# Performance work log

Measured on AMD Instinct MI355X. Metric: run time of the kernel, lower is better.

The kernel has to match this reference:

```python
import jax, jax.numpy as jnp
import numpy as np

B, S, D, H = 2, 2048, 1024, 16
DH = D // H  # 64, matches Attention's hardcoded d_k=64 scale


def setup_inputs() -> dict:
    key = jax.random.key(0)
    kq, kk, kv, kw, kb = jax.random.split(key, 5)
    return {
        "q": jax.random.normal(kq, (B, S, D), dtype=jnp.float32),
        "k": jax.random.normal(kk, (B, S, D), dtype=jnp.float32),
        "v": jax.random.normal(kv, (B, S, D), dtype=jnp.float32),
        "w_o_w": jax.random.normal(kw, (D, D), dtype=jnp.float32) * 0.02,
        "w_o_b": jax.random.normal(kb, (D,), dtype=jnp.float32) * 0.02,
    }


def _to_heads(x):
    # [B,S,D] -> [B,H,S,DH]
    b, s, d = x.shape
    return x.reshape(b, s, H, DH).transpose(0, 2, 1, 3)


def reference(q, k, v, w_o_w, w_o_b):
    # pre-activation (F.relu) on raw q,k,v
    qh = _to_heads(jax.nn.relu(q))
    kh = _to_heads(jax.nn.relu(k))
    vh = _to_heads(jax.nn.relu(v))
    scale = 1.0 / jnp.sqrt(jnp.asarray(DH, dtype=q.dtype))
    # naive attention: full [B,H,S,S] score matrix, softmax over keys
    scores = jnp.einsum("bhsd,bhtd->bhst", qh, kh) * scale
    probs = jax.nn.softmax(scores, axis=-1)
    attn = jnp.einsum("bhst,bhtd->bhsd", probs, vh)
    # merge heads: [B,H,S,DH] -> [B,S,D]
    out = attn.transpose(0, 2, 1, 3).reshape(B, S, D)
    # output projection (nn.Linear applies x @ W.T + b) then post-activation
    out = out @ w_o_w.T + w_o_b
    return jax.nn.relu(out)
```

## Files before the change

### kernel.cpp

```cpp
#include <hip/hip_runtime.h>
#include <hip/hip_bf16.h>

#define Bc 2
#define Hc 16
#define Sc 2048
#define Dc 1024

typedef __attribute__((ext_vector_type(8))) short s16x8;
typedef __attribute__((ext_vector_type(4))) float f32x4;
typedef __attribute__((ext_vector_type(16))) float f32x16;

#define AS1 __attribute__((address_space(1)))
#define AS3 __attribute__((address_space(3)))

static __device__ __forceinline__ int swz(int row) {
    return (row & 7) ^ ((row >> 3) & 3);
}

static __device__ __forceinline__ float fexp2(float x) {
#if __has_builtin(__builtin_amdgcn_exp2f)
    return __builtin_amdgcn_exp2f(x);
#else
    float r; asm("v_exp_f32 %0, %1" : "=v"(r) : "v"(x)); return r;
#endif
}

static __device__ __forceinline__ unsigned cvtpk(float lo, float hi) {
    unsigned r; asm("v_cvt_pk_bf16_f32 %0, %1, %2" : "=v"(r) : "v"(lo), "v"(hi));
    return r;
}

static __device__ __forceinline__ void plswap(unsigned &x, unsigned &y) {
#if __has_builtin(__builtin_amdgcn_permlane32_swap)
    typedef __attribute__((ext_vector_type(2))) unsigned int u32x2;
    u32x2 t = __builtin_amdgcn_permlane32_swap(x, y, false, false);
    x = t.x; y = t.y;
#else
    asm volatile("v_permlane32_swap_b32 %0, %1" : "+v"(x), "+v"(y));
#endif
}

static __device__ __forceinline__ unsigned short f2bf(float f) {
    union { float f; unsigned u; } x; x.f = f;
    unsigned r = x.u + 0x7fffu + ((x.u >> 16) & 1u);
    return (unsigned short)(r >> 16);
}

__global__ __launch_bounds__(256) void prep_all(const float* __restrict__ q,
                                                const float* __restrict__ k,
                                                const float* __restrict__ v,
                                                const float* __restrict__ w,
                                                unsigned short* __restrict__ qh,
                                                unsigned short* __restrict__ kh,
                                                unsigned short* __restrict__ vt,
                                                unsigned short* __restrict__ wb) {
    const int bid = blockIdx.x;
    const int tid = threadIdx.x;
    if (bid < 8192) {
        const bool isQ = bid < 4096;
        const float* src = isQ ? q : k;
        unsigned short* dst = isQ ? qh : kh;
        const float scale = isQ ? 0.18033688011112042f : 1.0f;
        long i = ((long)(bid & 4095) * 256 + tid) * 4;
        int dh = (int)(i & 63);
        int h  = (int)((i >> 6) & (Hc - 1));
        int s  = (int)((i >> 10) & (Sc - 1));
        int b  = (int)(i >> 21);
        float4 x = *reinterpret_cast<const float4*>(src + i);
        long o = (((long)b * Hc + h) * Sc + s) * 64 + dh;
        ushort4 r;
        r.x = f2bf(fmaxf(x.x, 0.f) * scale);
        r.y = f2bf(fmaxf(x.y, 0.f) * scale);
        r.z = f2bf(fmaxf(x.z, 0.f) * scale);
        r.w = f2bf(fmaxf(x.w, 0.f) * scale);
        *reinterpret_cast<ushort4*>(dst + o) = r;
    } else if (bid < 9216) {
        __shared__ unsigned short lds[64][66];
        const int lb = bid - 8192;
        const int st = lb & (Sc / 64 - 1);
        const int bh = lb >> 5;
        const int b = bh >> 4, h = bh & 15;
#pragma unroll
        for (int i = 0; i < 4; ++i) {
            int srow = (tid >> 4) + i * 16;
            int scol = (tid & 15) * 4;
            float4 x = *(const float4*)(v + ((long)b * Sc + st * 64 + srow) * Dc + h * 64 + scol);
            lds[srow][scol + 0] = f2bf(fmaxf(x.x, 0.f));
            lds[srow][scol + 1] = f2bf(fmaxf(x.y, 0.f));
            lds[srow][scol + 2] = f2bf(fmaxf(x.z, 0.f));
            lds[srow][scol + 3] = f2bf(fmaxf(x.w, 0.f));
        }
        __syncthreads();
#pragma unroll
        for (int i = 0; i < 2; ++i) {
            int dh = (tid >> 3) + i * 32;
            int sc = (tid & 7) * 8;
            union { unsigned short u[8]; s16x8 v8; } o;
#pragma unroll
            for (int j = 0; j < 8; ++j) o.u[j] = lds[sc + j][dh];
            *(s16x8*)(vt + ((long)bh * 64 + dh) * Sc + st * 64 + sc) = o.v8;
        }
    } else {
        const int lb = bid - 9216;
        long i = ((long)lb * 256 + tid) * 4;
        float4 x = *reinterpret_cast<const float4*>(w + i);
        ushort4 r;
        r.x = f2bf(x.x); r.y = f2bf(x.y); r.z = f2bf(x.z); r.w = f2bf(x.w);
        *reinterpret_cast<ushort4*>(wb + i) = r;
    }
}

__global__ __launch_bounds__(256, 2) void attn_lds(const unsigned short* __restrict__ qh,
                                                   const unsigned short* __restrict__ kh,
                                                   const unsigned short* __restrict__ vt,
                                                   unsigned short* __restrict__ xout) {
    __shared__ unsigned short Klds[2][64 * 64];
    __shared__ unsigned short Vlds[2][64 * 64];

    const int tid = threadIdx.x;
    const int l = tid & 63, w = tid >> 6;
    const int r32 = l & 31, hl = l >> 5;
    const int job = (blockIdx.x & 7) * 64 + (blockIdx.x >> 3);
    const int qb = job & 15;
    const int bh = job >> 4;
    const int phase = job & 31;

    const unsigned short* Qp = qh + ((long)bh * Sc + qb * 128 + w * 32) * 64;
    const unsigned short* Kp = kh + (long)bh * Sc * 64;
    const unsigned short* Vp = vt + (long)bh * 64 * Sc;

    s16x8 qbf[4];
#pragma unroll
    for (int ds = 0; ds < 4; ++ds)
        qbf[ds] = *(const s16x8*)(Qp + r32 * 64 + ds * 16 + hl * 8);

    f32x16 acc0 = {0,0,0,0,0,0,0,0,0,0,0,0,0,0,0,0};
    f32x16 acc1 = {0,0,0,0,0,0,0,0,0,0,0,0,0,0,0,0};
    float denom = 0.f;

    auto stage = [&](int buf, int kv0) {
#pragma unroll
        for (int j = 0; j < 2; ++j) {
            const int cbase = w * 64 + j * 256;
            const int chunk = cbase + l;
            const int row = chunk >> 3, cc = chunk & 7;
            const int scc = cc ^ swz(row);
            const unsigned short* ksrc = Kp + (long)(kv0 + row) * 64 + scc * 8;
            const unsigned short* vsrc = Vp + (long)row * Sc + kv0 + scc * 8;
            __builtin_amdgcn_global_load_lds((const AS1 unsigned int*)(const void*)ksrc,
                                             (AS3 unsigned int*)(void*)&Klds[buf][cbase * 8],
                                             16, 0, 0);
            __builtin_amdgcn_global_load_lds((const AS1 unsigned int*)(const void*)vsrc,
                                             (AS3 unsigned int*)(void*)&Vlds[buf][cbase * 8],
                                             16, 0, 0);
        }
    };

    auto compute = [&](int buf) {
        const unsigned short* KB = &Klds[buf][0];
        const unsigned short* VB = &Vlds[buf][0];
        unsigned Bw[4][4];
#pragma unroll
        for (int kt = 0; kt < 2; ++kt) {
            f32x16 st = {0,0,0,0,0,0,0,0,0,0,0,0,0,0,0,0};
#pragma unroll
            for (int ds = 0; ds < 4; ++ds) {
                const int row = kt * 32 + r32;
                const int cc = ((ds * 2 + hl) ^ swz(row));
                s16x8 ka = *(const s16x8*)(KB + row * 64 + cc * 8);
                st = __builtin_amdgcn_mfma_f32_32x32x16_bf16(ka, qbf[ds], st, 0, 0, 0);
            }
            float p[16];
#pragma unroll
            for (int i = 0; i < 16; ++i) p[i] = fexp2(st[i]);
            denom += (((p[0] + p[1]) + (p[2] + p[3])) + ((p[4] + p[5]) + (p[6] + p[7])))
                   + (((p[8] + p[9]) + (p[10] + p[11])) + ((p[12] + p[13]) + (p[14] + p[15])));
            unsigned a0 = cvtpk(p[0], p[1]),   b0 = cvtpk(p[2], p[3]);
            unsigned c0 = cvtpk(p[4], p[5]),   d0 = cvtpk(p[6], p[7]);
            unsigned a1 = cvtpk(p[8], p[9]),   b1 = cvtpk(p[10], p[11]);
            unsigned c1 = cvtpk(p[12], p[13]), d1 = cvtpk(p[14], p[15]);
            plswap(a0, c0); plswap(b0, d0);
            plswap(a1, c1); plswap(b1, d1);
            Bw[kt * 2 + 0][0] = a0; Bw[kt * 2 + 0][1] = b0;
            Bw[kt * 2 + 0][2] = c0; Bw[kt * 2 + 0][3] = d0;
            Bw[kt * 2 + 1][0] = a1; Bw[kt * 2 + 1][1] = b1;
            Bw[kt * 2 + 1][2] = c1; Bw[kt * 2 + 1][3] = d1;
        }
#pragma unroll
        for (int dt = 0; dt < 2; ++dt) {
#pragma unroll
            for (int s = 0; s < 4; ++s) {
                const int row = dt * 32 + r32;
                const int cc = ((s * 2 + hl) ^ swz(row));
                s16x8 va = *(const s16x8*)(VB + row * 64 + cc * 8);
                union { unsigned u[4]; s16x8 v8; } bp;
                bp.u[0] = Bw[s][0]; bp.u[1] = Bw[s][1];
                bp.u[2] = Bw[s][2]; bp.u[3] = Bw[s][3];
                if (dt == 0)
                    acc0 = __builtin_amdgcn_mfma_f32_32x32x16_bf16(va, bp.v8, acc0, 0, 0, 0);
                else
                    acc1 = __builtin_amdgcn_mfma_f32_32x32x16_bf16(va, bp.v8, acc1, 0, 0, 0);
            }
        }
    };

    stage(0, phase * 64);
    __syncthreads();
    int cur = 0;
    for (int t = 0; t < Sc / 64 - 1; ++t) {
        stage(cur ^ 1, ((t + 1 + phase) & (Sc / 64 - 1)) * 64);
        compute(cur);
        __syncthreads();
        cur ^= 1;
    }
    compute(cur);

    float dn = denom + __shfl_xor(denom, 32);
    const float inv = 1.0f / dn;
    const int b = bh >> 4, h = bh & 15;
    unsigned short* Xrow = xout + ((long)b * Sc + qb * 128 + w * 32 + r32) * Dc + h * 64;
#pragma unroll
    for (int dt = 0; dt < 2; ++dt) {
        const f32x16& A = dt ? acc1 : acc0;
#pragma unroll
        for (int rg = 0; rg < 4; ++rg) {
            unsigned wlo = cvtpk(A[rg * 4 + 0] * inv, A[rg * 4 + 1] * inv);
            unsigned whi = cvtpk(A[rg * 4 + 2] * inv, A[rg * 4 + 3] * inv);
            uint2 wv; wv.x = wlo; wv.y = whi;
            *reinterpret_cast<uint2*>(Xrow + dt * 32 + rg * 8 + hl * 4) = wv;
        }
    }
}

__global__ __launch_bounds__(256, 2) void proj256(const unsigned short* __restrict__ X,
                                                  const unsigned short* __restrict__ Wb,
                                                  const float* __restrict__ bias,
                                                  float* __restrict__ out) {
    __shared__ unsigned short Xlds[2][128 * 64];
    __shared__ unsigned short Wlds[2][128 * 64];

    const int tid = threadIdx.x;
    const int l = tid & 63, w = tid >> 6;
    const int r32 = l & 31, hl = l >> 5;
    const int job = (blockIdx.x & 7) * 32 + (blockIdx.x >> 3);
    const int nb = job & 7;
    const int mb = job >> 3;

    const unsigned short* Xp = X + (long)mb * 128 * Dc;
    const unsigned short* Wp = Wb + (long)nb * 128 * Dc;

    f32x16 acc[4];
#pragma unroll
    for (int nt = 0; nt < 4; ++nt)
        acc[nt] = (f32x16){0,0,0,0,0,0,0,0,0,0,0,0,0,0,0,0};

    auto stage = [&](int buf, int k0) {
#pragma unroll
        for (int j = 0; j < 4; ++j) {
            const int chunk = j * 256 + tid;
            const int row = chunk >> 3, cc = chunk & 7;
            const int scc = cc ^ swz(row);
            const unsigned short* xsrc = Xp + (long)row * Dc + k0 + scc * 8;
            const unsigned short* wsrc = Wp + (long)row * Dc + k0 + scc * 8;
            __builtin_amdgcn_global_load_lds((const AS1 unsigned int*)(const void*)xsrc,
                                             (AS3 unsigned int*)(void*)&Xlds[buf][chunk * 8],
                                             16, 0, 0);
            __builtin_amdgcn_global_load_lds((const AS1 unsigned int*)(const void*)wsrc,
                                             (AS3 unsigned int*)(void*)&Wlds[buf][chunk * 8],
                                             16, 0, 0);
        }
    };

    auto compute = [&](int buf) {
        const unsigned short* XB = &Xlds[buf][0];
        const unsigned short* WB = &Wlds[buf][0];
#pragma unroll
        for (int ks = 0; ks < 4; ++ks) {
            const int arow = w * 32 + r32;
            const int acc_ = ((ks * 2 + hl) ^ swz(arow));
            s16x8 af = *(const s16x8*)(XB + arow * 64 + acc_ * 8);
#pragma unroll
            for (int nt = 0; nt < 4; ++nt) {
                const int brow = nt * 32 + r32;
                const int bcc = ((ks * 2 + hl) ^ swz(brow));
                s16x8 bf = *(const s16x8*)(WB + brow * 64 + bcc * 8);
                acc[nt] = __builtin_amdgcn_mfma_f32_32x32x16_bf16(af, bf, acc[nt], 0, 0, 0);
            }
        }
    };

    stage(0, 0);
    __syncthreads();
    int cur = 0;
    for (int t = 0; t < Dc / 64 - 1; ++t) {
        stage(cur ^ 1, (t + 1) * 64);
        compute(cur);
        __syncthreads();
        cur ^= 1;
    }
    compute(cur);

#pragma unroll
    for (int nt = 0; nt < 4; ++nt) {
        const float bv = bias[nb * 128 + nt * 32 + r32];
#pragma unroll
        for (int j = 0; j < 16; ++j) {
            const int m = (j & 3) + 8 * (j >> 2) + 4 * hl;
            out[((long)(mb * 128 + w * 32 + m)) * Dc + nb * 128 + nt * 32 + r32] =
                fmaxf(acc[nt][j] + bv, 0.f);
        }
    }
}

extern "C" void kernel_launch(void* const* d_in, const int* in_sizes, int n_in,
                              void* d_out, int out_size, void* d_ws, size_t ws_size,
                              hipStream_t stream) {
    const float* q    = (const float*)d_in[0];
    const float* k    = (const float*)d_in[1];
    const float* v    = (const float*)d_in[2];
    const float* w    = (const float*)d_in[3];
    const float* bias = (const float*)d_in[4];
    float* out = (float*)d_out;

    unsigned short* ws = (unsigned short*)d_ws;
    unsigned short* qh = ws;
    unsigned short* kh = qh + 4194304;
    unsigned short* vt = kh + 4194304;
    unsigned short* wb = vt + 4194304;
    unsigned short* X  = wb + 1048576;

    prep_all<<<10240, 256, 0, stream>>>(q, k, v, w, qh, kh, vt, wb);
    attn_lds<<<Bc * Hc * (Sc / 128), 256, 0, stream>>>(qh, kh, vt, X);
    proj256<<<(Bc * Sc / 128) * (Dc / 128), 256, 0, stream>>>(X, wb, bias, out);
}
```

Before: 81.18 us.

## Split KV range across wave pairs in attention and merge partial outputs via LDS

The attention kernel now gives each block 64 query rows instead of 128 and doubles the grid. Each pair of waves shares a 32-row query tile and splits the KV sequence into two halves, each wave handling 32 keys per stage. Partial numerators and denominators are reduced through LDS at the end. The change also raises launch bounds to 4 blocks per CU and adds s_setprio around the MFMA sections. The aim is more parallelism and occupancy and less register pressure per wave, at the cost of staging K/V once per 64 queries instead of once per 128, which doubles K/V traffic, plus an extra LDS reduction.

```diff
diff --git a/kernel.cpp b/kernel.cpp
--- a/kernel.cpp
+++ b/kernel.cpp
@@ -110,22 +110,24 @@
     }
 }
 
-__global__ __launch_bounds__(256, 2) void attn_lds(const unsigned short* __restrict__ qh,
+__global__ __launch_bounds__(256, 4) void attn_skv(const unsigned short* __restrict__ qh,
                                                    const unsigned short* __restrict__ kh,
                                                    const unsigned short* __restrict__ vt,
                                                    unsigned short* __restrict__ xout) {
     __shared__ unsigned short Klds[2][64 * 64];
     __shared__ unsigned short Vlds[2][64 * 64];
+    __shared__ float dsm[4][32];
 
     const int tid = threadIdx.x;
     const int l = tid & 63, w = tid >> 6;
     const int r32 = l & 31, hl = l >> 5;
-    const int job = (blockIdx.x & 7) * 64 + (blockIdx.x >> 3);
-    const int qb = job & 15;
-    const int bh = job >> 4;
+    const int qi = w & 1, hf = w >> 1;
+    const int job = (blockIdx.x & 7) * 128 + (blockIdx.x >> 3);
+    const int qb = job & 31;
+    const int bh = job >> 5;
     const int phase = job & 31;
 
-    const unsigned short* Qp = qh + ((long)bh * Sc + qb * 128 + w * 32) * 64;
+    const unsigned short* Qp = qh + ((long)bh * Sc + qb * 64 + qi * 32) * 64;
     const unsigned short* Kp = kh + (long)bh * Sc * 64;
     const unsigned short* Vp = vt + (long)bh * 64 * Sc;
 
@@ -138,20 +140,29 @@
     f32x16 acc1 = {0,0,0,0,0,0,0,0,0,0,0,0,0,0,0,0};
     float denom = 0.f;
 
-    auto stage = [&](int buf, int kv0) {
+    auto stage = [&](int buf, int t) {
+        const int kvh0 = ((t + phase) & 31) * 32;
+        const int kvh1 = 1024 + kvh0;
 #pragma unroll
         for (int j = 0; j < 2; ++j) {
-            const int cbase = w * 64 + j * 256;
-            const int chunk = cbase + l;
+            const int chunk = j * 256 + tid;
             const int row = chunk >> 3, cc = chunk & 7;
             const int scc = cc ^ swz(row);
-            const unsigned short* ksrc = Kp + (long)(kv0 + row) * 64 + scc * 8;
-            const unsigned short* vsrc = Vp + (long)row * Sc + kv0 + scc * 8;
+            const int kvr = (row < 32) ? (kvh0 + row) : (kvh1 + row - 32);
+            const unsigned short* ksrc = Kp + (long)kvr * 64 + scc * 8;
             __builtin_amdgcn_global_load_lds((const AS1 unsigned int*)(const void*)ksrc,
-                                             (AS3 unsigned int*)(void*)&Klds[buf][cbase * 8],
+                                             (AS3 unsigned int*)(void*)&Klds[buf][chunk * 8],
                                              16, 0, 0);
+        }
+#pragma unroll
+        for (int j = 0; j < 2; ++j) {
+            const int chunk = j * 256 + tid;
+            const int row = chunk >> 3, cc = chunk & 7;
+            const int scc = cc ^ swz(row);
+            const int kvc = (scc < 4) ? (kvh0 + scc * 8) : (kvh1 + (scc - 4) * 8);
+            const unsigned short* vsrc = Vp + (long)row * Sc + kvc;
             __builtin_amdgcn_global_load_lds((const AS1 unsigned int*)(const void*)vsrc,
-                                             (AS3 unsigned int*)(void*)&Vlds[buf][cbase * 8],
+                                             (AS3 unsigned int*)(void*)&Vlds[buf][chunk * 8],
                                              16, 0, 0);
         }
     };
@@ -159,75 +170,94 @@
     auto compute = [&](int buf) {
         const unsigned short* KB = &Klds[buf][0];
         const unsigned short* VB = &Vlds[buf][0];
-        unsigned Bw[4][4];
-#pragma unroll
-        for (int kt = 0; kt < 2; ++kt) {
-            f32x16 st = {0,0,0,0,0,0,0,0,0,0,0,0,0,0,0,0};
-#pragma unroll
-            for (int ds = 0; ds < 4; ++ds) {
-                const int row = kt * 32 + r32;
-                const int cc = ((ds * 2 + hl) ^ swz(row));
-                s16x8 ka = *(const s16x8*)(KB + row * 64 + cc * 8);
-                st = __builtin_amdgcn_mfma_f32_32x32x16_bf16(ka, qbf[ds], st, 0, 0, 0);
-            }
-            float p[16];
-#pragma unroll
-            for (int i = 0; i < 16; ++i) p[i] = fexp2(st[i]);
-            denom += (((p[0] + p[1]) + (p[2] + p[3])) + ((p[4] + p[5]) + (p[6] + p[7])))
-                   + (((p[8] + p[9]) + (p[10] + p[11])) + ((p[12] + p[13]) + (p[14] + p[15])));
-            unsigned a0 = cvtpk(p[0], p[1]),   b0 = cvtpk(p[2], p[3]);
-            unsigned c0 = cvtpk(p[4], p[5]),   d0 = cvtpk(p[6], p[7]);
-            unsigned a1 = cvtpk(p[8], p[9]),   b1 = cvtpk(p[10], p[11]);
-            unsigned c1 = cvtpk(p[12], p[13]), d1 = cvtpk(p[14], p[15]);
-            plswap(a0, c0); plswap(b0, d0);
-            plswap(a1, c1); plswap(b1, d1);
-            Bw[kt * 2 + 0][0] = a0; Bw[kt * 2 + 0][1] = b0;
-            Bw[kt * 2 + 0][2] = c0; Bw[kt * 2 + 0][3] = d0;
-            Bw[kt * 2 + 1][0] = a1; Bw[kt * 2 + 1][1] = b1;
-            Bw[kt * 2 + 1][2] = c1; Bw[kt * 2 + 1][3] = d1;
-        }
-#pragma unroll
-        for (int dt = 0; dt < 2; ++dt) {
-#pragma unroll
-            for (int s = 0; s < 4; ++s) {
+        f32x16 st = {0,0,0,0,0,0,0,0,0,0,0,0,0,0,0,0};
+        const int krow = hf * 32 + r32;
+        __builtin_amdgcn_s_setprio(1);
+#pragma unroll
+        for (int ds = 0; ds < 4; ++ds) {
+            const int cc = ((ds * 2 + hl) ^ swz(krow));
+            s16x8 ka = *(const s16x8*)(KB + krow * 64 + cc * 8);
+            st = __builtin_amdgcn_mfma_f32_32x32x16_bf16(ka, qbf[ds], st, 0, 0, 0);
+        }
+        __builtin_amdgcn_s_setprio(0);
+        float p[16];
+#pragma unroll
+        for (int i = 0; i < 16; ++i) p[i] = fexp2(st[i]);
+        denom += (((p[0] + p[1]) + (p[2] + p[3])) + ((p[4] + p[5]) + (p[6] + p[7])))
+               + (((p[8] + p[9]) + (p[10] + p[11])) + ((p[12] + p[13]) + (p[14] + p[15])));
+        unsigned a0 = cvtpk(p[0], p[1]),   b0 = cvtpk(p[2], p[3]);
+        unsigned c0 = cvtpk(p[4], p[5]),   d0 = cvtpk(p[6], p[7]);
+        unsigned a1 = cvtpk(p[8], p[9]),   b1 = cvtpk(p[10], p[11]);
+        unsigned c1 = cvtpk(p[12], p[13]), d1 = cvtpk(p[14], p[15]);
+        plswap(a0, c0); plswap(b0, d0);
+        plswap(a1, c1); plswap(b1, d1);
+        unsigned Bw[2][4] = {{a0, b0, c0, d0}, {a1, b1, c1, d1}};
+        __builtin_amdgcn_s_setprio(1);
+#pragma unroll
+        for (int ks = 0; ks < 2; ++ks) {
+            union { unsigned u[4]; s16x8 v8; } bp;
+            bp.u[0] = Bw[ks][0]; bp.u[1] = Bw[ks][1];
+            bp.u[2] = Bw[ks][2]; bp.u[3] = Bw[ks][3];
+#pragma unroll
+            for (int dt = 0; dt < 2; ++dt) {
                 const int row = dt * 32 + r32;
-                const int cc = ((s * 2 + hl) ^ swz(row));
+                const int lc = hf * 4 + ks * 2 + hl;
+                const int cc = (lc ^ swz(row));
                 s16x8 va = *(const s16x8*)(VB + row * 64 + cc * 8);
-                union { unsigned u[4]; s16x8 v8; } bp;
-                bp.u[0] = Bw[s][0]; bp.u[1] = Bw[s][1];
-                bp.u[2] = Bw[s][2]; bp.u[3] = Bw[s][3];
                 if (dt == 0)
                     acc0 = __builtin_amdgcn_mfma_f32_32x32x16_bf16(va, bp.v8, acc0, 0, 0, 0);
                 else
                     acc1 = __builtin_amdgcn_mfma_f32_32x32x16_bf16(va, bp.v8, acc1, 0, 0, 0);
             }
         }
+        __builtin_amdgcn_s_setprio(0);
     };
 
-    stage(0, phase * 64);
+    stage(0, 0);
     __syncthreads();
     int cur = 0;
-    for (int t = 0; t < Sc / 64 - 1; ++t) {
-        stage(cur ^ 1, ((t + 1 + phase) & (Sc / 64 - 1)) * 64);
+    for (int t = 0; t < 31; ++t) {
+        stage(cur ^ 1, t + 1);
         compute(cur);
         __syncthreads();
         cur ^= 1;
     }
     compute(cur);
 
-    float dn = denom + __shfl_xor(denom, 32);
-    const float inv = 1.0f / dn;
-    const int b = bh >> 4, h = bh & 15;
-    unsigned short* Xrow = xout + ((long)b * Sc + qb * 128 + w * 32 + r32) * Dc + h * 64;
-#pragma unroll
-    for (int dt = 0; dt < 2; ++dt) {
-        const f32x16& A = dt ? acc1 : acc0;
-#pragma unroll
-        for (int rg = 0; rg < 4; ++rg) {
-            unsigned wlo = cvtpk(A[rg * 4 + 0] * inv, A[rg * 4 + 1] * inv);
-            unsigned whi = cvtpk(A[rg * 4 + 2] * inv, A[rg * 4 + 3] * inv);
-            uint2 wv; wv.x = wlo; wv.y = whi;
-            *reinterpret_cast<uint2*>(Xrow + dt * 32 + rg * 8 + hl * 4) = wv;
+    float dnw = denom + __shfl_xor(denom, 32);
+    __syncthreads();
+    float* mg0 = (float*)&Klds[0][0];
+    float* mg1 = (float*)&Vlds[0][0];
+    float* dst = (w < 2) ? (mg0 + w * 2048) : (mg1 + (w - 2) * 2048);
+#pragma unroll
+    for (int rg = 0; rg < 16; ++rg) {
+        dst[rg * 64 + l]        = acc0[rg];
+        dst[1024 + rg * 64 + l] = acc1[rg];
+    }
+    if (l < 32) dsm[w][l] = dnw;
+    __syncthreads();
+
+    if (w < 2) {
+        const float dn = dsm[w][r32] + dsm[w + 2][r32];
+        const float inv = 1.0f / dn;
+        const float* pa = mg0 + w * 2048;
+        const float* pb = mg1 + w * 2048;
+        const int b = bh >> 4, h = bh & 15;
+        unsigned short* Xrow = xout + ((long)b * Sc + qb * 64 + w * 32 + r32) * Dc + h * 64;
+#pragma unroll
+        for (int dt = 0; dt < 2; ++dt) {
+#pragma unroll
+            for (int rg = 0; rg < 4; ++rg) {
+                const int base = dt * 1024 + rg * 4 * 64 + l;
+                float o0 = pa[base]       + pb[base];
+                float o1 = pa[base + 64]  + pb[base + 64];
+                float o2 = pa[base + 128] + pb[base + 128];
+                float o3 = pa[base + 192] + pb[base + 192];
+                unsigned wlo = cvtpk(o0 * inv, o1 * inv);
+                unsigned whi = cvtpk(o2 * inv, o3 * inv);
+                uint2 wv; wv.x = wlo; wv.y = whi;
+                *reinterpret_cast<uint2*>(Xrow + dt * 32 + rg * 8 + hl * 4) = wv;
+            }
         }
     }
 }
@@ -330,6 +360,6 @@
     unsigned short* X  = wb + 1048576;
 
     prep_all<<<10240, 256, 0, stream>>>(q, k, v, w, qh, kh, vt, wb);
-    attn_lds<<<Bc * Hc * (Sc / 128), 256, 0, stream>>>(qh, kh, vt, X);
+    attn_skv<<<Bc * Hc * (Sc / 64), 256, 0, stream>>>(qh, kh, vt, X);
     proj256<<<(Bc * Sc / 128) * (Dc / 128), 256, 0, stream>>>(X, wb, bias, out);
 }
```

Result: slower. 85.48 us (+5.3%).
